# Performance work log

Hardware: AMD Instinct MI355X
Metric: run time of the kernel (lower is better)

## Reference

```python
import jax, jax.numpy as jnp
import numpy as np

D_MODEL, D_K, D_V, HEADS = 512, 8, 8, 6
EPS = 1e-5


def setup_inputs() -> dict:
    key = jax.random.key(0)
    ks = jax.random.split(key, 16)
    B, S = 16, 1024
    inp = {
        'q_input': jax.random.normal(ks[0], (B, S, D_MODEL), jnp.float32),
        'k_input': jax.random.normal(ks[1], (B, S, D_MODEL), jnp.float32),
        'v_input': jax.random.normal(ks[2], (B, S, D_MODEL), jnp.float32),
        'mask': jax.random.randint(ks[3], (B, S, S), 0, 2).astype(bool),
        'Wq': jax.random.normal(ks[4], (D_MODEL, D_K * HEADS), jnp.float32) * 0.04,
        'bq': jax.random.normal(ks[5], (D_K * HEADS,), jnp.float32) * 0.02,
        'Wk': jax.random.normal(ks[6], (D_MODEL, D_K * HEADS), jnp.float32) * 0.04,
        'bk': jax.random.normal(ks[7], (D_K * HEADS,), jnp.float32) * 0.02,
        'Wv': jax.random.normal(ks[8], (D_MODEL, D_V * HEADS), jnp.float32) * 0.04,
        'bv': jax.random.normal(ks[9], (D_V * HEADS,), jnp.float32) * 0.02,
        'Wo': jax.random.normal(ks[10], (HEADS * D_K, D_MODEL), jnp.float32) * 0.1,
        'bo': jax.random.normal(ks[11], (D_MODEL,), jnp.float32) * 0.02,
        'ln_w': 1.0 + jax.random.normal(ks[12], (D_MODEL,), jnp.float32) * 0.02,
        'ln_b': jax.random.normal(ks[13], (D_MODEL,), jnp.float32) * 0.02,
    }
    return inp


def reference(q_input, k_input, v_input, mask, Wq, bq, Wk, bk, Wv, bv, Wo, bo, ln_w, ln_b):
    B, S, _ = q_input.shape
    # projections -> [B, H, S, d]
    q_s = (q_input @ Wq + bq).reshape(B, S, HEADS, D_K).transpose(0, 2, 1, 3)
    k_s = (k_input @ Wk + bk).reshape(B, S, HEADS, D_K).transpose(0, 2, 1, 3)
    v_s = (v_input @ Wv + bv).reshape(B, S, HEADS, D_V).transpose(0, 2, 1, 3)
    # scaled dot-product with masked_fill(mask, 1e-9) as in the original (fills VALUE, not -inf)
    scores = jnp.einsum('bhqd,bhkd->bhqk', q_s, k_s) / np.sqrt(D_K).astype(np.float32)
    scores = jnp.where(mask[:, None, :, :], jnp.float32(1e-9), scores)
    attn = jax.nn.softmax(scores, axis=-1)
    out = jnp.einsum('bhqk,bhkd->bhqd', attn, v_s)  # [B,H,S,d_v]
    out = out.transpose(0, 2, 1, 3).reshape(B, S, HEADS * D_K)
    out = out @ Wo + bo
    x = q_input + out  # residual
    mu = jnp.mean(x, axis=-1, keepdims=True)
    var = jnp.var(x, axis=-1, keepdims=True)
    return (x - mu) * jax.lax.rsqrt(var + EPS) * ln_w + ln_b
```

## Files before the change

kernel.cpp:

```cpp
#include <hip/hip_runtime.h>

constexpr int B = 16;
constexpr int S = 1024;
constexpr int DM = 512;
constexpr int H = 6;
constexpr int DK = 8;
constexpr int NJ = H * DK;
constexpr int BS = B * S;
constexpr int WB_ELEMS = 16 * NJ * 32;

typedef __attribute__((ext_vector_type(8))) short bf16x8;
typedef __attribute__((ext_vector_type(4))) float floatx4;

#define LOG2E 1.4426950408889634f
#define QSCALE (0.35355339059327373f * LOG2E)
#define MASKVAL (1e-9f * LOG2E)

__device__ inline ushort f2bf(float f) {
  unsigned int u = __builtin_bit_cast(unsigned int, f);
  return (ushort)((u + 0x7FFFu + ((u >> 16) & 1u)) >> 16);
}

__global__ __launch_bounds__(256) void maskbits_kernel(
    const int* __restrict__ mask, unsigned long long* __restrict__ bits) {
  int wave = threadIdx.x >> 6, lane = threadIdx.x & 63;
  int row = blockIdx.x * 4 + wave;
  const int* mrow = mask + (size_t)row * S;
  unsigned long long* brow = bits + (size_t)row * 16;
#pragma unroll
  for (int c = 0; c < 16; c++) {
    int v = mrow[c * 64 + lane];
    unsigned long long bal = __ballot(v != 0);
    if (lane == 0) brow[c] = bal;
  }
}

__global__ __launch_bounds__(256) void wprep_kernel(
    const float* __restrict__ Wq, const float* __restrict__ Wk,
    const float* __restrict__ Wv, ushort* __restrict__ Wb) {
  int m = blockIdx.x;
  const float* W = (m == 0) ? Wq : (m == 1) ? Wk : Wv;
  ushort* dst = Wb + (size_t)m * WB_ELEMS;
  for (int e = threadIdx.x; e < WB_ELEMS; e += 256) {
    int kc = e >> 11;
    kc = e / 1536;
    int rem = e - kc * 1536;
    int n = rem >> 5, kj = rem & 31;
    dst[e] = f2bf(W[(size_t)(kc * 32 + kj) * NJ + n]);
  }
}

__global__ __launch_bounds__(256) void proj_kernel(
    const float* __restrict__ q_in, const float* __restrict__ k_in,
    const float* __restrict__ v_in, const ushort* __restrict__ Wb,
    const float* __restrict__ bq, const float* __restrict__ bk,
    const float* __restrict__ bv,
    ushort* __restrict__ Qo, ushort* __restrict__ Ko, ushort* __restrict__ Vo) {
  int m = blockIdx.y;
  const float* x    = (m == 0) ? q_in : (m == 1) ? k_in : v_in;
  const float* bias = (m == 0) ? bq   : (m == 1) ? bk   : bv;
  ushort* out       = (m == 0) ? Qo   : (m == 1) ? Ko   : Vo;
  float oscale      = (m == 0) ? QSCALE : 1.0f;
  const ushort* Wg  = Wb + (size_t)m * WB_ELEMS;

  __shared__ ushort Wl[WB_ELEMS];

  int t = threadIdx.x;
  {
    const uint4* src = (const uint4*)Wg;
    uint4* dst = (uint4*)Wl;
#pragma unroll
    for (int i = 0; i < 12; i++) dst[t + i * 256] = src[t + i * 256];
  }

  int r0 = blockIdx.x * 64;
  int wave = t >> 6, lane = t & 63;
  int n16 = lane & 15, quad = lane >> 4;
  const float* xrow = x + (size_t)(r0 + wave * 16 + n16) * DM + quad * 8;

  floatx4 acc0 = {0.f, 0.f, 0.f, 0.f};
  floatx4 acc1 = {0.f, 0.f, 0.f, 0.f};
  floatx4 acc2 = {0.f, 0.f, 0.f, 0.f};

  __syncthreads();

#pragma unroll 4
  for (int kc = 0; kc < 16; kc++) {
    float4 xa = *(const float4*)(xrow + kc * 32);
    float4 xb = *(const float4*)(xrow + kc * 32 + 4);
    bf16x8 a;
    a[0] = (short)f2bf(xa.x); a[1] = (short)f2bf(xa.y);
    a[2] = (short)f2bf(xa.z); a[3] = (short)f2bf(xa.w);
    a[4] = (short)f2bf(xb.x); a[5] = (short)f2bf(xb.y);
    a[6] = (short)f2bf(xb.z); a[7] = (short)f2bf(xb.w);
    const ushort* wbase = &Wl[(kc * 48 + n16) * 32 + quad * 8];
    bf16x8 b0 = *(const bf16x8*)(wbase);
    bf16x8 b1 = *(const bf16x8*)(wbase + 16 * 32);
    bf16x8 b2 = *(const bf16x8*)(wbase + 32 * 32);
    acc0 = __builtin_amdgcn_mfma_f32_16x16x32_bf16(a, b0, acc0, 0, 0, 0);
    acc1 = __builtin_amdgcn_mfma_f32_16x16x32_bf16(a, b1, acc1, 0, 0, 0);
    acc2 = __builtin_amdgcn_mfma_f32_16x16x32_bf16(a, b2, acc2, 0, 0, 0);
  }

  int baseR = r0 + wave * 16 + quad * 4;
#pragma unroll
  for (int j = 0; j < 3; j++) {
    floatx4 a = (j == 0) ? acc0 : (j == 1) ? acc1 : acc2;
    int n = j * 16 + n16;
    float bn = bias[n];
    int h = n >> 3, d = n & 7;
#pragma unroll
    for (int r = 0; r < 4; r++) {
      int R = baseR + r;
      int b = R >> 10, s = R & 1023;
      out[(((size_t)(b * H + h)) * S + s) * 8 + d] = f2bf((a[r] + bn) * oscale);
    }
  }
}

__global__ __launch_bounds__(256) void attn_kernel(
    const ushort* __restrict__ Qg, const ushort* __restrict__ Kg,
    const ushort* __restrict__ Vg, const unsigned long long* __restrict__ bits,
    float* __restrict__ A) {
  int bh = blockIdx.x >> 4;
  int qt = blockIdx.x & 15;
  int b = bh / H, h = bh % H;
  int q0 = qt * 64;

  __shared__ ushort Ks[1024 * 8];
  __shared__ ushort Vt[9 * 1032];
  __shared__ unsigned long long Mw[64 * 16];
  __shared__ uint Pb[4][2][16 * 20];

  int t = threadIdx.x;
  int wave = t >> 6, lane = t & 63;
  int quad = lane >> 4, n16 = lane & 15;

  const ushort* Kbase = Kg + (size_t)bh * S * 8;
  const ushort* Vbase = Vg + (size_t)bh * S * 8;
  const unsigned long long* Bbase = bits + ((size_t)(b * S + q0)) * 16;

#pragma unroll
  for (int i = 0; i < 4; i++) {
    int e = t + i * 256;
    *(uint4*)&Ks[e * 8] = *(const uint4*)&Kbase[e * 8];
  }
#pragma unroll
  for (int i = 0; i < 8; i++) {
    int e = t + i * 256;
    int key = e >> 1, db = (e & 1) << 2;
    ushort4 v = *(const ushort4*)&Vbase[key * 8 + db];
    int g = (key & ~31) + 2 * (key & 15) + ((key >> 4) & 1);
    Vt[(db + 0) * 1032 + g] = v.x;
    Vt[(db + 1) * 1032 + g] = v.y;
    Vt[(db + 2) * 1032 + g] = v.z;
    Vt[(db + 3) * 1032 + g] = v.w;
  }
#pragma unroll
  for (int i = 0; i < 4; i++) Vt[8 * 1032 + t + i * 256] = 0x3F80;
#pragma unroll
  for (int i = 0; i < 4; i++) Mw[t + i * 256] = Bbase[t + i * 256];
  __syncthreads();

  bf16x8 aq = {0, 0, 0, 0, 0, 0, 0, 0};
  if (quad == 0)
    aq = *(const bf16x8*)&Qg[((size_t)bh * S + q0 + wave * 16 + n16) * 8];

  floatx4 acc = {0.f, 0.f, 0.f, 0.f};
  const floatx4 zero = {0.f, 0.f, 0.f, 0.f};

#pragma unroll 2
  for (int c = 0; c < 32; c++) {
    bf16x8 bk0 = *(const bf16x8*)&Ks[(c * 32 + n16) * 8];
    bf16x8 bk1 = *(const bf16x8*)&Ks[(c * 32 + 16 + n16) * 8];
    floatx4 sc0 = __builtin_amdgcn_mfma_f32_16x16x32_bf16(aq, bk0, zero, 0, 0, 0);
    floatx4 sc1 = __builtin_amdgcn_mfma_f32_16x16x32_bf16(aq, bk1, zero, 0, 0, 0);

    int basebit = (c & 1) * 32;
    int wi = c >> 1;
    uint* prow = &Pb[wave][c & 1][0];
#pragma unroll
    for (int r = 0; r < 4; r++) {
      unsigned long long mw = Mw[(wave * 16 + quad * 4 + r) * 16 + wi];
      float s0 = ((mw >> (basebit + n16)) & 1ull) ? MASKVAL : sc0[r];
      float s1 = ((mw >> (basebit + 16 + n16)) & 1ull) ? MASKVAL : sc1[r];
      float p0 = exp2f(fminf(s0, 80.f));
      float p1 = exp2f(fminf(s1, 80.f));
      uint pw = (uint)f2bf(p0) | ((uint)f2bf(p1) << 16);
      prow[(quad * 4 + r) * 20 + n16] = pw;
    }

    bf16x8 ap = *(const bf16x8*)((const ushort*)prow + n16 * 40 + quad * 8);
    int dd = (n16 < 9) ? n16 : 8;
    bf16x8 bv = *(const bf16x8*)&Vt[dd * 1032 + c * 32 + quad * 8];
    acc = __builtin_amdgcn_mfma_f32_16x16x32_bf16(ap, bv, acc, 0, 0, 0);
  }

#pragma unroll
  for (int r = 0; r < 4; r++) {
    float dnm = __shfl(acc[r], (lane & 48) | 8, 64);
    if (n16 < 8) {
      int qg = q0 + wave * 16 + quad * 4 + r;
      A[((size_t)(b * S + qg)) * NJ + h * 8 + n16] = acc[r] / dnm;
    }
  }
}

__global__ __launch_bounds__(256) void out_ln_kernel(
    const float* __restrict__ A, const float* __restrict__ Wo,
    const float* __restrict__ bo, const float* __restrict__ qin,
    const float* __restrict__ lnw, const float* __restrict__ lnb,
    float* __restrict__ out) {
  int r0 = blockIdx.x * 8;
  int t = threadIdx.x;
  __shared__ float As[8 * NJ];
#pragma unroll
  for (int i = t; i < 8 * NJ; i += 256) As[i] = A[(size_t)r0 * NJ + i];
  __syncthreads();

  int c0 = t, c1 = t + 256;
  float acc0[8], acc1[8];
#pragma unroll
  for (int r = 0; r < 8; r++) { acc0[r] = 0.f; acc1[r] = 0.f; }

#pragma unroll 4
  for (int j = 0; j < NJ; j++) {
    float w0 = Wo[(size_t)j * DM + c0];
    float w1 = Wo[(size_t)j * DM + c1];
#pragma unroll
    for (int r = 0; r < 8; r++) {
      float a = As[r * NJ + j];
      acc0[r] += a * w0;
      acc1[r] += a * w1;
    }
  }

  float b0 = bo[c0], b1 = bo[c1];
  float y0[8], y1[8], ssum[8], sq[8];
#pragma unroll
  for (int r = 0; r < 8; r++) {
    y0[r] = acc0[r] + b0 + qin[(size_t)(r0 + r) * DM + c0];
    y1[r] = acc1[r] + b1 + qin[(size_t)(r0 + r) * DM + c1];
    ssum[r] = y0[r] + y1[r];
    sq[r] = y0[r] * y0[r] + y1[r] * y1[r];
  }

  int wave = t >> 6, lane = t & 63;
  __shared__ float reds[4][8], redq[4][8];
#pragma unroll
  for (int r = 0; r < 8; r++) {
    float s = ssum[r], qq = sq[r];
#pragma unroll
    for (int off = 32; off > 0; off >>= 1) {
      s += __shfl_xor(s, off, 64);
      qq += __shfl_xor(qq, off, 64);
    }
    if (lane == 0) { reds[wave][r] = s; redq[wave][r] = qq; }
  }
  __syncthreads();

  float lw0 = lnw[c0], lw1 = lnw[c1], lb0 = lnb[c0], lb1 = lnb[c1];
#pragma unroll
  for (int r = 0; r < 8; r++) {
    float s = (reds[0][r] + reds[1][r]) + (reds[2][r] + reds[3][r]);
    float qq = (redq[0][r] + redq[1][r]) + (redq[2][r] + redq[3][r]);
    float mu = s * (1.f / 512.f);
    float var = qq * (1.f / 512.f) - mu * mu;
    float rstd = rsqrtf(var + 1e-5f);
    out[(size_t)(r0 + r) * DM + c0] = (y0[r] - mu) * rstd * lw0 + lb0;
    out[(size_t)(r0 + r) * DM + c1] = (y1[r] - mu) * rstd * lw1 + lb1;
  }
}

extern "C" void kernel_launch(void* const* d_in, const int* in_sizes, int n_in,
                              void* d_out, int out_size, void* d_ws,
                              size_t ws_size, hipStream_t stream) {
  const float* q_in = (const float*)d_in[0];
  const float* k_in = (const float*)d_in[1];
  const float* v_in = (const float*)d_in[2];
  const int* mask = (const int*)d_in[3];
  const float* Wq = (const float*)d_in[4];
  const float* bq = (const float*)d_in[5];
  const float* Wk = (const float*)d_in[6];
  const float* bk = (const float*)d_in[7];
  const float* Wv = (const float*)d_in[8];
  const float* bv = (const float*)d_in[9];
  const float* Wo = (const float*)d_in[10];
  const float* bo = (const float*)d_in[11];
  const float* lnw = (const float*)d_in[12];
  const float* lnb = (const float*)d_in[13];
  float* out = (float*)d_out;

  constexpr size_t QKV = (size_t)B * H * S * DK;
  ushort* base = (ushort*)d_ws;
  ushort* Qw = base;
  ushort* Kw = base + QKV;
  ushort* Vw = base + 2 * QKV;
  float* Aw = (float*)(base + 3 * QKV);
  unsigned long long* bits = (unsigned long long*)(Aw + (size_t)BS * NJ);
  ushort* Wb = (ushort*)(bits + (size_t)BS * 16);

  maskbits_kernel<<<BS / 4, 256, 0, stream>>>(mask, bits);
  wprep_kernel<<<3, 256, 0, stream>>>(Wq, Wk, Wv, Wb);
  proj_kernel<<<dim3(BS / 64, 3), 256, 0, stream>>>(
      q_in, k_in, v_in, Wb, bq, bk, bv, Qw, Kw, Vw);
  attn_kernel<<<(B * H * S) / 64, 256, 0, stream>>>(Qw, Kw, Vw, bits, Aw);
  out_ln_kernel<<<BS / 8, 256, 0, stream>>>(Aw, Wo, bo, q_in, lnw, lnb, out);
}
```

Measured before the change: 316.6 us.

## Use fp16 P·V MFMA with bitwise mask select and vectorized mask-word loads

V is now stored as fp16, and the attention probabilities are packed with cvt_pkrtz into fp16 for a 16x16x32 f16 MFMA. The per-element branchy 64-bit mask test is replaced by a bitwise select that writes 1.0 (0x3C00) for masked keys. Mask words are now staged as padded 32-bit rows and read four at a time as uint4. The exp2 clamp drops to 15 to stay inside fp16 range, and the P staging buffer loses its double buffering. These changes aim to cut ALU and LDS work in the softmax loop, but they change rounding and would saturate any large scores.

```diff
diff --git a/kernel.cpp b/kernel.cpp
--- a/kernel.cpp
+++ b/kernel.cpp
@@ -10,11 +10,11 @@
 constexpr int WB_ELEMS = 16 * NJ * 32;
 
 typedef __attribute__((ext_vector_type(8))) short bf16x8;
+typedef __attribute__((ext_vector_type(8))) _Float16 half8;
 typedef __attribute__((ext_vector_type(4))) float floatx4;
 
 #define LOG2E 1.4426950408889634f
 #define QSCALE (0.35355339059327373f * LOG2E)
-#define MASKVAL (1e-9f * LOG2E)
 
 __device__ inline ushort f2bf(float f) {
   unsigned int u = __builtin_bit_cast(unsigned int, f);
@@ -42,8 +42,7 @@
   const float* W = (m == 0) ? Wq : (m == 1) ? Wk : Wv;
   ushort* dst = Wb + (size_t)m * WB_ELEMS;
   for (int e = threadIdx.x; e < WB_ELEMS; e += 256) {
-    int kc = e >> 11;
-    kc = e / 1536;
+    int kc = e / 1536;
     int rem = e - kc * 1536;
     int n = rem >> 5, kj = rem & 31;
     dst[e] = f2bf(W[(size_t)(kc * 32 + kj) * NJ + n]);
@@ -113,15 +112,18 @@
     for (int r = 0; r < 4; r++) {
       int R = baseR + r;
       int b = R >> 10, s = R & 1023;
-      out[(((size_t)(b * H + h)) * S + s) * 8 + d] = f2bf((a[r] + bn) * oscale);
+      float fv = (a[r] + bn) * oscale;
+      ushort val = (m == 2) ? __builtin_bit_cast(ushort, (_Float16)fv)
+                            : f2bf(fv);
+      out[(((size_t)(b * H + h)) * S + s) * 8 + d] = val;
     }
   }
 }
 
 __global__ __launch_bounds__(256) void attn_kernel(
     const ushort* __restrict__ Qg, const ushort* __restrict__ Kg,
-    const ushort* __restrict__ Vg, const unsigned long long* __restrict__ bits,
-    float* __restrict__ A) {
+    const ushort* __restrict__ Vg ,
+    const uint* __restrict__ bits32, float* __restrict__ A) {
   int bh = blockIdx.x >> 4;
   int qt = blockIdx.x & 15;
   int b = bh / H, h = bh % H;
@@ -129,8 +131,8 @@
 
   __shared__ ushort Ks[1024 * 8];
   __shared__ ushort Vt[9 * 1032];
-  __shared__ unsigned long long Mw[64 * 16];
-  __shared__ uint Pb[4][2][16 * 20];
+  __shared__ uint Mw[64 * 36];
+  __shared__ uint Pb[4][16 * 20];
 
   int t = threadIdx.x;
   int wave = t >> 6, lane = t & 63;
@@ -138,7 +140,7 @@
 
   const ushort* Kbase = Kg + (size_t)bh * S * 8;
   const ushort* Vbase = Vg + (size_t)bh * S * 8;
-  const unsigned long long* Bbase = bits + ((size_t)(b * S + q0)) * 16;
+  const uint* Bbase = bits32 + ((size_t)(b * S + q0)) * 32;
 
 #pragma unroll
   for (int i = 0; i < 4; i++) {
@@ -157,9 +159,13 @@
     Vt[(db + 3) * 1032 + g] = v.w;
   }
 #pragma unroll
-  for (int i = 0; i < 4; i++) Vt[8 * 1032 + t + i * 256] = 0x3F80;
-#pragma unroll
-  for (int i = 0; i < 4; i++) Mw[t + i * 256] = Bbase[t + i * 256];
+  for (int i = 0; i < 4; i++) Vt[8 * 1032 + t + i * 256] = 0x3C00;
+#pragma unroll
+  for (int i = 0; i < 8; i++) {
+    int e = t + i * 256;
+    int row = e >> 5, w = e & 31;
+    Mw[row * 36 + w] = Bbase[row * 32 + w];
+  }
   __syncthreads();
 
   bf16x8 aq = {0, 0, 0, 0, 0, 0, 0, 0};
@@ -168,32 +174,42 @@
 
   floatx4 acc = {0.f, 0.f, 0.f, 0.f};
   const floatx4 zero = {0.f, 0.f, 0.f, 0.f};
-
-#pragma unroll 2
-  for (int c = 0; c < 32; c++) {
-    bf16x8 bk0 = *(const bf16x8*)&Ks[(c * 32 + n16) * 8];
-    bf16x8 bk1 = *(const bf16x8*)&Ks[(c * 32 + 16 + n16) * 8];
-    floatx4 sc0 = __builtin_amdgcn_mfma_f32_16x16x32_bf16(aq, bk0, zero, 0, 0, 0);
-    floatx4 sc1 = __builtin_amdgcn_mfma_f32_16x16x32_bf16(aq, bk1, zero, 0, 0, 0);
-
-    int basebit = (c & 1) * 32;
-    int wi = c >> 1;
-    uint* prow = &Pb[wave][c & 1][0];
-#pragma unroll
-    for (int r = 0; r < 4; r++) {
-      unsigned long long mw = Mw[(wave * 16 + quad * 4 + r) * 16 + wi];
-      float s0 = ((mw >> (basebit + n16)) & 1ull) ? MASKVAL : sc0[r];
-      float s1 = ((mw >> (basebit + 16 + n16)) & 1ull) ? MASKVAL : sc1[r];
-      float p0 = exp2f(fminf(s0, 80.f));
-      float p1 = exp2f(fminf(s1, 80.f));
-      uint pw = (uint)f2bf(p0) | ((uint)f2bf(p1) << 16);
-      prow[(quad * 4 + r) * 20 + n16] = pw;
-    }
-
-    bf16x8 ap = *(const bf16x8*)((const ushort*)prow + n16 * 40 + quad * 8);
-    int dd = (n16 < 9) ? n16 : 8;
-    bf16x8 bv = *(const bf16x8*)&Vt[dd * 1032 + c * 32 + quad * 8];
-    acc = __builtin_amdgcn_mfma_f32_16x16x32_bf16(ap, bv, acc, 0, 0, 0);
+  int row0 = wave * 16 + quad * 4;
+  uint* prow = &Pb[wave][0];
+
+#pragma unroll 1
+  for (int cc = 0; cc < 8; cc++) {
+    uint4 mr[4];
+#pragma unroll
+    for (int r = 0; r < 4; r++)
+      mr[r] = *(const uint4*)&Mw[(row0 + r) * 36 + cc * 4];
+
+#pragma unroll
+    for (int ci = 0; ci < 4; ci++) {
+      int c = cc * 4 + ci;
+      bf16x8 bk0 = *(const bf16x8*)&Ks[(c * 32 + n16) * 8];
+      bf16x8 bk1 = *(const bf16x8*)&Ks[(c * 32 + 16 + n16) * 8];
+      floatx4 sc0 = __builtin_amdgcn_mfma_f32_16x16x32_bf16(aq, bk0, zero, 0, 0, 0);
+      floatx4 sc1 = __builtin_amdgcn_mfma_f32_16x16x32_bf16(aq, bk1, zero, 0, 0, 0);
+
+#pragma unroll
+      for (int r = 0; r < 4; r++) {
+        uint mw = (ci == 0) ? mr[r].x : (ci == 1) ? mr[r].y
+                : (ci == 2) ? mr[r].z : mr[r].w;
+        uint tt = mw >> n16;
+        uint mexp = (tt & 0x10001u) * 0xFFFFu;
+        float p0 = exp2f(fminf(sc0[r], 15.f));
+        float p1 = exp2f(fminf(sc1[r], 15.f));
+        uint pw = __builtin_bit_cast(uint, __builtin_amdgcn_cvt_pkrtz(p0, p1));
+        pw = (mexp & 0x3C003C00u) | (~mexp & pw);
+        prow[(quad * 4 + r) * 20 + n16] = pw;
+      }
+
+      half8 ap = *(const half8*)((const ushort*)prow + n16 * 40 + quad * 8);
+      int dd = (n16 < 9) ? n16 : 8;
+      half8 bv = *(const half8*)&Vt[dd * 1032 + c * 32 + quad * 8];
+      acc = __builtin_amdgcn_mfma_f32_16x16x32_f16(ap, bv, acc, 0, 0, 0);
+    }
   }
 
 #pragma unroll
@@ -304,6 +320,7 @@
   wprep_kernel<<<3, 256, 0, stream>>>(Wq, Wk, Wv, Wb);
   proj_kernel<<<dim3(BS / 64, 3), 256, 0, stream>>>(
       q_in, k_in, v_in, Wb, bq, bk, bv, Qw, Kw, Vw);
-  attn_kernel<<<(B * H * S) / 64, 256, 0, stream>>>(Qw, Kw, Vw, bits, Aw);
+  attn_kernel<<<(B * H * S) / 64, 256, 0, stream>>>(
+      Qw, Kw, Vw, (const uint*)bits, Aw);
   out_ln_kernel<<<BS / 8, 256, 0, stream>>>(Aw, Wo, bo, q_in, lnw, lnb, out);
 }
```

Measured after the change: 310.4 us. -2.0%, faster.
